# Optimization experiments

Hardware: AMD Instinct MI355X
Metric: run time of the kernel (lower is better)

## Reference

```python
import jax, jax.numpy as jnp
import numpy as np


def setup_inputs() -> dict:
    key = jax.random.key(0)
    k1, k2, k3 = jax.random.split(key, 3)
    B, S, Q, K, D = 64, 512, 800, 4, 64
    q_data = jax.random.normal(k1, (B, S, Q), dtype=jnp.float32)
    r_data = jax.random.randint(k2, (B, S), 0, K)
    # learned params (xavier-ish scale)
    Wq = jax.random.normal(k3, (D, Q), dtype=jnp.float32) * (0.5 * (2.0 / (Q + D)) ** 0.5)
    bq = jnp.zeros((D,), dtype=jnp.float32)
    Wr = jax.random.normal(jax.random.fold_in(key, 7), (1, K), dtype=jnp.float32) * (0.5 * (2.0 / (K + 1)) ** 0.5)
    br = jnp.zeros((1,), dtype=jnp.float32)
    return {"q_data": q_data, "r_data": r_data, "Wq": Wq, "bq": bq,
            "Wr": Wr, "br": br, "n_questions": Q, "n_cats": K}


def reference(q_data, r_data, Wq, bq, Wr, br, n_questions, n_cats):
    # Vectorized over (batch, seq): original looped over t in python.
    K = n_cats
    k_idx = jnp.arange(K, dtype=q_data.dtype)                      # [K]
    dist = jnp.abs(k_idx[None, None, :] - r_data[..., None].astype(q_data.dtype)) / (K - 1)  # [B,S,K]
    weights = jnp.maximum(1.0 - dist, 0.0)                        # [B,S,K]
    # response_weights: Linear(K -> 1) then sigmoid -> scalar gate per (b,s)
    gate = jax.nn.sigmoid(jnp.einsum('bsk,ok->bso', weights, Wr) + br)  # [B,S,1]
    weighted_q = q_data * gate                                    # [B,S,Q]
    # question_embed: Linear(Q -> D)
    out = jnp.einsum('bsq,dq->bsd', weighted_q, Wq) + bq          # [B,S,D]
    return out
```

## Files before the change

kernel.cpp:

```cpp
#include <hip/hip_runtime.h>
#include <hip/hip_bf16.h>


#define QD 800
#define DD 64
#define M_TOTAL 32768
#define KT 25
#define KSPLIT 13
#define DEPTH 3

typedef __attribute__((ext_vector_type(8))) short bf16x8;
typedef __attribute__((ext_vector_type(4))) float f32x4;

static __device__ __forceinline__ short f2bf(float f) {
  union { __hip_bfloat16 h; short s; } u;
  u.h = __float2bfloat16(f);
  return u.s;
}

static __device__ __forceinline__ bf16x8 pack8(f32x4 lo, f32x4 hi) {
  bf16x8 r;
  r[0] = f2bf(lo.x); r[1] = f2bf(lo.y); r[2] = f2bf(lo.z); r[3] = f2bf(lo.w);
  r[4] = f2bf(hi.x); r[5] = f2bf(hi.y); r[6] = f2bf(hi.z); r[7] = f2bf(hi.w);
  return r;
}

static __device__ __forceinline__ bf16x8 load_split8(const float* __restrict__ p) {
  return pack8(*reinterpret_cast<const f32x4*>(p),
               *reinterpret_cast<const f32x4*>(p + 16));
}

__global__ void convert_wq_kernel(const float* __restrict__ Wq, short* __restrict__ Bb) {
  int idx = blockIdx.x * 256 + threadIdx.x;
  int kt = idx >> 8;
  int c = (idx >> 6) & 3;
  int lane = idx & 63;
  int l15 = lane & 15, lhi = lane >> 4;
  const float* p = Wq + (c * 16 + l15) * QD + kt * 32 + lhi * 4;
  *reinterpret_cast<bf16x8*>(Bb + (size_t)idx * 8) = load_split8(p);
}

template <int CNT>
static __device__ __forceinline__ void pipe_loop(
    const float* __restrict__ a0, const float* __restrict__ a1,
    const float* __restrict__ a2, const float* __restrict__ a3,
    const short* __restrict__ bp, f32x4 (&acc)[4][4]) {
  const float* at[4] = {a0, a1, a2, a3};
  f32x4 sAlo[DEPTH][4], sAhi[DEPTH][4];
  bf16x8 sB[DEPTH][4];

#pragma unroll
  for (int s = 0; s < DEPTH; ++s) {
    if (s < CNT) {
#pragma unroll
      for (int t = 0; t < 4; ++t) {
        sAlo[s][t] = *reinterpret_cast<const f32x4*>(at[t] + s * 32);
        sAhi[s][t] = *reinterpret_cast<const f32x4*>(at[t] + s * 32 + 16);
      }
#pragma unroll
      for (int c = 0; c < 4; ++c)
        sB[s][c] = *reinterpret_cast<const bf16x8*>(bp + s * 2048 + c * 512);
    }
  }

#pragma unroll
  for (int kt = 0; kt < CNT; ++kt) {
    const int s = kt % DEPTH;
    bf16x8 afr[4];
#pragma unroll
    for (int t = 0; t < 4; ++t) afr[t] = pack8(sAlo[s][t], sAhi[s][t]);
#pragma unroll
    for (int t = 0; t < 4; ++t)
#pragma unroll
      for (int c = 0; c < 4; ++c)
        acc[t][c] = __builtin_amdgcn_mfma_f32_16x16x32_bf16(afr[t], sB[s][c],
                                                            acc[t][c], 0, 0, 0);
    const int nx = kt + DEPTH;
    if (nx < CNT) {
#pragma unroll
      for (int t = 0; t < 4; ++t) {
        sAlo[s][t] = *reinterpret_cast<const f32x4*>(at[t] + nx * 32);
        sAhi[s][t] = *reinterpret_cast<const f32x4*>(at[t] + nx * 32 + 16);
      }
#pragma unroll
      for (int c = 0; c < 4; ++c)
        sB[s][c] = *reinterpret_cast<const bf16x8*>(bp + nx * 2048 + c * 512);
    }
    __builtin_amdgcn_sched_barrier(0);
  }
}

__global__ __launch_bounds__(128, 1) void sold_kernel(
    const float* __restrict__ q, const int* __restrict__ rdat,
    const short* __restrict__ Bb, const float* __restrict__ bq,
    const float* __restrict__ Wr, const float* __restrict__ br,
    float* __restrict__ out) {
  const int lane = threadIdx.x & 63;
  const int khalf = threadIdx.x >> 6;
  const int l15 = lane & 15;
  const int lhi = lane >> 4;
  const int m0 = blockIdx.x * 64;
  const int kt0 = khalf ? KSPLIT : 0;

  const float* a0 = q + (size_t)(m0 +  0 + l15) * QD + kt0 * 32 + lhi * 4;
  const float* a1 = q + (size_t)(m0 + 16 + l15) * QD + kt0 * 32 + lhi * 4;
  const float* a2 = q + (size_t)(m0 + 32 + l15) * QD + kt0 * 32 + lhi * 4;
  const float* a3 = q + (size_t)(m0 + 48 + l15) * QD + kt0 * 32 + lhi * 4;
  const short* bp = Bb + (size_t)kt0 * 2048 + lane * 8;

  f32x4 acc[4][4];
#pragma unroll
  for (int t = 0; t < 4; ++t)
#pragma unroll
    for (int c = 0; c < 4; ++c) acc[t][c] = {0.f, 0.f, 0.f, 0.f};

  if (khalf == 0) {
    pipe_loop<KSPLIT>(a0, a1, a2, a3, bp, acc);
  } else {
    pipe_loop<KT - KSPLIT>(a0, a1, a2, a3, bp, acc);
  }

  __shared__ float comb[4][16][64];
  if (khalf == 1) {
#pragma unroll
    for (int t = 0; t < 4; ++t)
#pragma unroll
      for (int c = 0; c < 4; ++c)
#pragma unroll
        for (int r = 0; r < 4; ++r) comb[t][c * 4 + r][lane] = acc[t][c][r];
  }
  __syncthreads();
  if (khalf == 1) return;

#pragma unroll
  for (int t = 0; t < 4; ++t)
#pragma unroll
    for (int c = 0; c < 4; ++c)
#pragma unroll
      for (int r = 0; r < 4; ++r) acc[t][c][r] += comb[t][c * 4 + r][lane];

  float wr[4] = {Wr[0], Wr[1], Wr[2], Wr[3]};
  float brv = br[0];
  float lut[4];
  const float inv3 = 1.0f / 3.0f;
#pragma unroll
  for (int r = 0; r < 4; ++r) {
    float s = brv;
#pragma unroll
    for (int k = 0; k < 4; ++k)
      s += fmaxf(1.0f - fabsf((float)(k - r)) * inv3, 0.0f) * wr[k];
    lut[r] = 1.0f / (1.0f + __expf(-s));
  }

  float bqv[4];
#pragma unroll
  for (int c = 0; c < 4; ++c) bqv[c] = bq[c * 16 + l15];

#pragma unroll
  for (int t = 0; t < 4; ++t) {
#pragma unroll
    for (int r = 0; r < 4; ++r) {
      int row = m0 + t * 16 + lhi * 4 + r;
      float g = lut[rdat[row]];
      float* orow = out + (size_t)row * DD + l15;
#pragma unroll
      for (int c = 0; c < 4; ++c) orow[c * 16] = acc[t][c][r] * g + bqv[c];
    }
  }
}

__global__ __launch_bounds__(256, 2) void sold_direct(
    const float* __restrict__ q, const int* __restrict__ rdat,
    const float* __restrict__ Wq, const float* __restrict__ bq,
    const float* __restrict__ Wr, const float* __restrict__ br,
    float* __restrict__ out) {
  const int lane = threadIdx.x & 63;
  const int wave = threadIdx.x >> 6;
  const int l15 = lane & 15;
  const int lhi = lane >> 4;
  const int m0 = blockIdx.x * 64 + wave * 16;
  const float* aptr = q + (size_t)(m0 + l15) * QD + lhi * 4;
  const float* w0 = Wq + (0 * 16 + l15) * QD + lhi * 4;
  const float* w1 = Wq + (1 * 16 + l15) * QD + lhi * 4;
  const float* w2 = Wq + (2 * 16 + l15) * QD + lhi * 4;
  const float* w3 = Wq + (3 * 16 + l15) * QD + lhi * 4;
  f32x4 acc0 = {0.f,0.f,0.f,0.f}, acc1 = {0.f,0.f,0.f,0.f};
  f32x4 acc2 = {0.f,0.f,0.f,0.f}, acc3 = {0.f,0.f,0.f,0.f};
#pragma unroll 5
  for (int kt = 0; kt < KT; ++kt) {
    bf16x8 a  = load_split8(aptr + kt * 32);
    bf16x8 b0 = load_split8(w0 + kt * 32);
    bf16x8 b1 = load_split8(w1 + kt * 32);
    bf16x8 b2 = load_split8(w2 + kt * 32);
    bf16x8 b3 = load_split8(w3 + kt * 32);
    acc0 = __builtin_amdgcn_mfma_f32_16x16x32_bf16(a, b0, acc0, 0, 0, 0);
    acc1 = __builtin_amdgcn_mfma_f32_16x16x32_bf16(a, b1, acc1, 0, 0, 0);
    acc2 = __builtin_amdgcn_mfma_f32_16x16x32_bf16(a, b2, acc2, 0, 0, 0);
    acc3 = __builtin_amdgcn_mfma_f32_16x16x32_bf16(a, b3, acc3, 0, 0, 0);
  }
  float wr[4] = {Wr[0], Wr[1], Wr[2], Wr[3]};
  float brv = br[0], lut[4];
  const float inv3 = 1.0f / 3.0f;
#pragma unroll
  for (int r = 0; r < 4; ++r) {
    float s = brv;
#pragma unroll
    for (int k = 0; k < 4; ++k)
      s += fmaxf(1.0f - fabsf((float)(k - r)) * inv3, 0.0f) * wr[k];
    lut[r] = 1.0f / (1.0f + __expf(-s));
  }
  float bqv0 = bq[l15], bqv1 = bq[16 + l15], bqv2 = bq[32 + l15], bqv3 = bq[48 + l15];
#pragma unroll
  for (int r = 0; r < 4; ++r) {
    int row = m0 + lhi * 4 + r;
    float g = lut[rdat[row]];
    float* orow = out + (size_t)row * DD + l15;
    orow[0]  = acc0[r] * g + bqv0;
    orow[16] = acc1[r] * g + bqv1;
    orow[32] = acc2[r] * g + bqv2;
    orow[48] = acc3[r] * g + bqv3;
  }
}

extern "C" void kernel_launch(void* const* d_in, const int* in_sizes, int n_in,
                              void* d_out, int out_size, void* d_ws, size_t ws_size,
                              hipStream_t stream) {
  const float* q    = (const float*)d_in[0];
  const int*   rdat = (const int*)d_in[1];
  const float* Wq   = (const float*)d_in[2];
  const float* bq   = (const float*)d_in[3];
  const float* Wr   = (const float*)d_in[4];
  const float* br   = (const float*)d_in[5];
  float* out = (float*)d_out;

  const size_t need_ws = (size_t)KT * 2048 * sizeof(short);
  if (ws_size >= need_ws) {
    short* Bb = (short*)d_ws;
    convert_wq_kernel<<<KT, 256, 0, stream>>>(Wq, Bb);
    sold_kernel<<<M_TOTAL / 64, 128, 0, stream>>>(q, rdat, Bb, bq, Wr, br, out);
  } else {
    sold_direct<<<M_TOTAL / 64, 256, 0, stream>>>(q, rdat, Wq, bq, Wr, br, out);
  }
}
```

Before: 171.2 us.

## Stage bf16 Wq in LDS via global_load_lds and use 128-row blocks

The whole pre-converted bf16 Wq (100 KB) is loaded once per block into shared memory with direct global-to-LDS loads. Blocks are enlarged to 256 threads covering 128 rows, with four waves arranged as two row tiles by two K halves. B fragments are then read from LDS with double buffering, and the A prefetch depth drops from 3 to 2. This aims to cut repeated global/L2 reads of the weights and to raise parallelism per block. In exchange it pays a 100 KB LDS fill on every block and adds a sync before the main loop, and the large LDS footprint limits occupancy to about one block per CU.

```diff
diff --git a/kernel.cpp b/kernel.cpp
--- a/kernel.cpp
+++ b/kernel.cpp
@@ -1,16 +1,26 @@
 #include <hip/hip_runtime.h>
 #include <hip/hip_bf16.h>
+#include <stdint.h>
 
 
 #define QD 800
 #define DD 64
 #define M_TOTAL 32768
 #define KT 25
-#define KSPLIT 13
-#define DEPTH 3
+#define KH0 13
+#define KH1 12
+#define DEPTH 2
 
 typedef __attribute__((ext_vector_type(8))) short bf16x8;
 typedef __attribute__((ext_vector_type(4))) float f32x4;
+
+typedef const __attribute__((address_space(1))) uint32_t* gas1_u32;
+typedef __attribute__((address_space(3))) uint32_t* las3_u32;
+
+static __device__ __forceinline__ void gll16(const void* g, const void* l) {
+  __builtin_amdgcn_global_load_lds((gas1_u32)(uintptr_t)g,
+                                   (las3_u32)(uint32_t)(uintptr_t)l, 16, 0, 0);
+}
 
 static __device__ __forceinline__ short f2bf(float f) {
   union { __hip_bfloat16 h; short s; } u;
@@ -41,103 +51,128 @@
 }
 
 template <int CNT>
-static __device__ __forceinline__ void pipe_loop(
+static __device__ __forceinline__ void kh_loop(
     const float* __restrict__ a0, const float* __restrict__ a1,
     const float* __restrict__ a2, const float* __restrict__ a3,
-    const short* __restrict__ bp, f32x4 (&acc)[4][4]) {
-  const float* at[4] = {a0, a1, a2, a3};
-  f32x4 sAlo[DEPTH][4], sAhi[DEPTH][4];
-  bf16x8 sB[DEPTH][4];
+    const short* __restrict__ bb,
+    f32x4 (&acc)[4][4]) {
+  f32x4 sLo[DEPTH][4], sHi[DEPTH][4];
+  bf16x8 bB[2][4];
 
 #pragma unroll
   for (int s = 0; s < DEPTH; ++s) {
-    if (s < CNT) {
-#pragma unroll
-      for (int t = 0; t < 4; ++t) {
-        sAlo[s][t] = *reinterpret_cast<const f32x4*>(at[t] + s * 32);
-        sAhi[s][t] = *reinterpret_cast<const f32x4*>(at[t] + s * 32 + 16);
-      }
+    sLo[s][0] = *reinterpret_cast<const f32x4*>(a0 + s * 32);
+    sHi[s][0] = *reinterpret_cast<const f32x4*>(a0 + s * 32 + 16);
+    sLo[s][1] = *reinterpret_cast<const f32x4*>(a1 + s * 32);
+    sHi[s][1] = *reinterpret_cast<const f32x4*>(a1 + s * 32 + 16);
+    sLo[s][2] = *reinterpret_cast<const f32x4*>(a2 + s * 32);
+    sHi[s][2] = *reinterpret_cast<const f32x4*>(a2 + s * 32 + 16);
+    sLo[s][3] = *reinterpret_cast<const f32x4*>(a3 + s * 32);
+    sHi[s][3] = *reinterpret_cast<const f32x4*>(a3 + s * 32 + 16);
+  }
+#pragma unroll
+  for (int c = 0; c < 4; ++c)
+    bB[0][c] = *reinterpret_cast<const bf16x8*>(bb + c * 512);
+
+#pragma unroll
+  for (int i = 0; i < CNT; ++i) {
+    const int s = i & 1;
+    if (i + 1 < CNT) {
 #pragma unroll
       for (int c = 0; c < 4; ++c)
-        sB[s][c] = *reinterpret_cast<const bf16x8*>(bp + s * 2048 + c * 512);
-    }
-  }
-
-#pragma unroll
-  for (int kt = 0; kt < CNT; ++kt) {
-    const int s = kt % DEPTH;
-    bf16x8 afr[4];
-#pragma unroll
-    for (int t = 0; t < 4; ++t) afr[t] = pack8(sAlo[s][t], sAhi[s][t]);
-#pragma unroll
-    for (int t = 0; t < 4; ++t)
-#pragma unroll
-      for (int c = 0; c < 4; ++c)
-        acc[t][c] = __builtin_amdgcn_mfma_f32_16x16x32_bf16(afr[t], sB[s][c],
-                                                            acc[t][c], 0, 0, 0);
-    const int nx = kt + DEPTH;
-    if (nx < CNT) {
-#pragma unroll
-      for (int t = 0; t < 4; ++t) {
-        sAlo[s][t] = *reinterpret_cast<const f32x4*>(at[t] + nx * 32);
-        sAhi[s][t] = *reinterpret_cast<const f32x4*>(at[t] + nx * 32 + 16);
-      }
-#pragma unroll
-      for (int c = 0; c < 4; ++c)
-        sB[s][c] = *reinterpret_cast<const bf16x8*>(bp + nx * 2048 + c * 512);
+        bB[(i + 1) & 1][c] =
+            *reinterpret_cast<const bf16x8*>(bb + (i + 1) * 2048 + c * 512);
+    }
+    bf16x8 af0 = pack8(sLo[s][0], sHi[s][0]);
+    bf16x8 af1 = pack8(sLo[s][1], sHi[s][1]);
+    bf16x8 af2 = pack8(sLo[s][2], sHi[s][2]);
+    bf16x8 af3 = pack8(sLo[s][3], sHi[s][3]);
+#pragma unroll
+    for (int c = 0; c < 4; ++c) {
+      acc[0][c] = __builtin_amdgcn_mfma_f32_16x16x32_bf16(af0, bB[i & 1][c], acc[0][c], 0, 0, 0);
+      acc[1][c] = __builtin_amdgcn_mfma_f32_16x16x32_bf16(af1, bB[i & 1][c], acc[1][c], 0, 0, 0);
+      acc[2][c] = __builtin_amdgcn_mfma_f32_16x16x32_bf16(af2, bB[i & 1][c], acc[2][c], 0, 0, 0);
+      acc[3][c] = __builtin_amdgcn_mfma_f32_16x16x32_bf16(af3, bB[i & 1][c], acc[3][c], 0, 0, 0);
+    }
+    if (i + DEPTH < CNT) {
+      sLo[s][0] = *reinterpret_cast<const f32x4*>(a0 + (i + DEPTH) * 32);
+      sHi[s][0] = *reinterpret_cast<const f32x4*>(a0 + (i + DEPTH) * 32 + 16);
+      sLo[s][1] = *reinterpret_cast<const f32x4*>(a1 + (i + DEPTH) * 32);
+      sHi[s][1] = *reinterpret_cast<const f32x4*>(a1 + (i + DEPTH) * 32 + 16);
+      sLo[s][2] = *reinterpret_cast<const f32x4*>(a2 + (i + DEPTH) * 32);
+      sHi[s][2] = *reinterpret_cast<const f32x4*>(a2 + (i + DEPTH) * 32 + 16);
+      sLo[s][3] = *reinterpret_cast<const f32x4*>(a3 + (i + DEPTH) * 32);
+      sHi[s][3] = *reinterpret_cast<const f32x4*>(a3 + (i + DEPTH) * 32 + 16);
     }
     __builtin_amdgcn_sched_barrier(0);
   }
 }
 
-__global__ __launch_bounds__(128, 1) void sold_kernel(
+__global__ __launch_bounds__(256, 2) void sold_kernel(
     const float* __restrict__ q, const int* __restrict__ rdat,
     const short* __restrict__ Bb, const float* __restrict__ bq,
     const float* __restrict__ Wr, const float* __restrict__ br,
     float* __restrict__ out) {
-  const int lane = threadIdx.x & 63;
-  const int khalf = threadIdx.x >> 6;
+  const int t = threadIdx.x;
+  const int lane = t & 63;
+  const int wave = t >> 6;
+  const int rt = wave & 1;
+  const int kh = wave >> 1;
   const int l15 = lane & 15;
   const int lhi = lane >> 4;
-  const int m0 = blockIdx.x * 64;
-  const int kt0 = khalf ? KSPLIT : 0;
-
-  const float* a0 = q + (size_t)(m0 +  0 + l15) * QD + kt0 * 32 + lhi * 4;
-  const float* a1 = q + (size_t)(m0 + 16 + l15) * QD + kt0 * 32 + lhi * 4;
-  const float* a2 = q + (size_t)(m0 + 32 + l15) * QD + kt0 * 32 + lhi * 4;
-  const float* a3 = q + (size_t)(m0 + 48 + l15) * QD + kt0 * 32 + lhi * 4;
-  const short* bp = Bb + (size_t)kt0 * 2048 + lane * 8;
+  const int m0 = blockIdx.x * 128;
+
+  __shared__ __align__(16) char smem[102400];
+  short* Bs = (short*)smem;
+
+#pragma unroll 5
+  for (int iter = 0; iter < 25; ++iter) {
+    int chunk = iter * 256 + wave * 64;
+    gll16(Bb + (size_t)(chunk + lane) * 8, Bs + (size_t)chunk * 8);
+  }
+  __syncthreads();
+
+  const int kt0 = kh ? KH0 : 0;
+  const int rowb = m0 + rt * 64 + l15;
+  const float* a0 = q + (size_t)(rowb +  0) * QD + kt0 * 32 + lhi * 4;
+  const float* a1 = q + (size_t)(rowb + 16) * QD + kt0 * 32 + lhi * 4;
+  const float* a2 = q + (size_t)(rowb + 32) * QD + kt0 * 32 + lhi * 4;
+  const float* a3 = q + (size_t)(rowb + 48) * QD + kt0 * 32 + lhi * 4;
+  const short* bb = Bs + (size_t)kt0 * 2048 + lane * 8;
 
   f32x4 acc[4][4];
 #pragma unroll
-  for (int t = 0; t < 4; ++t)
-#pragma unroll
-    for (int c = 0; c < 4; ++c) acc[t][c] = {0.f, 0.f, 0.f, 0.f};
-
-  if (khalf == 0) {
-    pipe_loop<KSPLIT>(a0, a1, a2, a3, bp, acc);
+  for (int t4 = 0; t4 < 4; ++t4)
+#pragma unroll
+    for (int c = 0; c < 4; ++c) acc[t4][c] = {0.f, 0.f, 0.f, 0.f};
+
+  if (kh == 0) {
+    kh_loop<KH0>(a0, a1, a2, a3, bb, acc);
   } else {
-    pipe_loop<KT - KSPLIT>(a0, a1, a2, a3, bp, acc);
-  }
-
-  __shared__ float comb[4][16][64];
-  if (khalf == 1) {
-#pragma unroll
-    for (int t = 0; t < 4; ++t)
+    kh_loop<KH1>(a0, a1, a2, a3, bb, acc);
+  }
+
+  __syncthreads();
+  float* comb = (float*)smem;
+  if (kh == 1) {
+#pragma unroll
+    for (int t4 = 0; t4 < 4; ++t4)
 #pragma unroll
       for (int c = 0; c < 4; ++c)
 #pragma unroll
-        for (int r = 0; r < 4; ++r) comb[t][c * 4 + r][lane] = acc[t][c][r];
+        for (int r = 0; r < 4; ++r)
+          comb[(((rt * 4 + t4) * 16) + c * 4 + r) * 64 + lane] = acc[t4][c][r];
   }
   __syncthreads();
-  if (khalf == 1) return;
-
-#pragma unroll
-  for (int t = 0; t < 4; ++t)
+  if (kh == 1) return;
+
+#pragma unroll
+  for (int t4 = 0; t4 < 4; ++t4)
 #pragma unroll
     for (int c = 0; c < 4; ++c)
 #pragma unroll
-      for (int r = 0; r < 4; ++r) acc[t][c][r] += comb[t][c * 4 + r][lane];
+      for (int r = 0; r < 4; ++r)
+        acc[t4][c][r] += comb[(((rt * 4 + t4) * 16) + c * 4 + r) * 64 + lane];
 
   float wr[4] = {Wr[0], Wr[1], Wr[2], Wr[3]};
   float brv = br[0];
@@ -157,14 +192,14 @@
   for (int c = 0; c < 4; ++c) bqv[c] = bq[c * 16 + l15];
 
 #pragma unroll
-  for (int t = 0; t < 4; ++t) {
+  for (int t4 = 0; t4 < 4; ++t4) {
 #pragma unroll
     for (int r = 0; r < 4; ++r) {
-      int row = m0 + t * 16 + lhi * 4 + r;
+      int row = m0 + rt * 64 + t4 * 16 + lhi * 4 + r;
       float g = lut[rdat[row]];
       float* orow = out + (size_t)row * DD + l15;
 #pragma unroll
-      for (int c = 0; c < 4; ++c) orow[c * 16] = acc[t][c][r] * g + bqv[c];
+      for (int c = 0; c < 4; ++c) orow[c * 16] = acc[t4][c][r] * g + bqv[c];
     }
   }
 }
@@ -237,7 +272,7 @@
   if (ws_size >= need_ws) {
     short* Bb = (short*)d_ws;
     convert_wq_kernel<<<KT, 256, 0, stream>>>(Wq, Bb);
-    sold_kernel<<<M_TOTAL / 64, 128, 0, stream>>>(q, rdat, Bb, bq, Wr, br, out);
+    sold_kernel<<<M_TOTAL / 128, 256, 0, stream>>>(q, rdat, Bb, bq, Wr, br, out);
   } else {
     sold_direct<<<M_TOTAL / 64, 256, 0, stream>>>(q, rdat, Wq, bq, Wr, br, out);
   }
```

Result: no change. 173.0 us (+1.1%).
